# Optimization experiments

Hardware: AMD Instinct MI355X
Metric: run time of the kernel (lower is better)

Reference implementation:

```python
import jax, jax.numpy as jnp
import numpy as np

VOCAB, EMBED, H = 32000, 128, 128
B, T = 32, 2048


def setup_inputs() -> dict:
    key = jax.random.key(0)
    ks = jax.random.split(key, 8)
    tokens = jax.random.randint(ks[0], (B, T), 0, VOCAB, dtype=jnp.int32)
    emb = jax.random.normal(ks[1], (VOCAB, EMBED), jnp.float32) * 0.05
    # layer 0: input EMBED -> H ; layer 1: H -> H
    Wx0 = jax.random.normal(ks[2], (EMBED, H), jnp.float32) * (1.0 / np.sqrt(EMBED))
    Wh0 = jax.random.normal(ks[3], (H, H), jnp.float32) * (1.0 / np.sqrt(H))
    b0 = jnp.zeros((H,), jnp.float32)
    Wx1 = jax.random.normal(ks[4], (H, H), jnp.float32) * (1.0 / np.sqrt(H))
    Wh1 = jax.random.normal(ks[5], (H, H), jnp.float32) * (1.0 / np.sqrt(H))
    b1 = jnp.zeros((H,), jnp.float32)
    return {"tokens": tokens, "emb": emb, "Wx0": Wx0, "Wh0": Wh0, "b0": b0,
            "Wx1": Wx1, "Wh1": Wh1, "b1": b1}


def _simple_rnn(x, mask, Wx, Wh, b):
    # x: [B,T,Din], mask: [B,T] bool. Keras masked-step semantics: at masked
    # steps, state (== output for SimpleRNN) carries over unchanged.
    xt = jnp.swapaxes(x, 0, 1)                 # [T,B,Din]
    xproj = xt @ Wx + b                        # precompute input projection [T,B,H]
    mt = jnp.swapaxes(mask, 0, 1)[..., None]   # [T,B,1]
    h0 = jnp.zeros((x.shape[0], Wh.shape[0]), x.dtype)

    def step(h, inp):
        xp, m = inp
        h_new = jnp.tanh(xp + h @ Wh)
        h = jnp.where(m, h_new, h)
        return h, h

    _, ys = jax.lax.scan(step, h0, (xproj, mt))
    return jnp.swapaxes(ys, 0, 1)              # [B,T,H]


def reference(tokens, emb, Wx0, Wh0, b0, Wx1, Wh1, b1):
    mask = tokens != 0                          # mask_zero=True
    x = emb[tokens]                             # [B,T,E]
    x = _simple_rnn(x, mask, Wx0, Wh0, b0)
    x = _simple_rnn(x, mask, Wx1, Wh1, b1)
    return x
```

## Files before the change

### kernel.cpp

```cpp
#include <hip/hip_runtime.h>
#include <math.h>

#define BB 32
#define TT 2048
#define HH 128

#define LDS_BARRIER() asm volatile("s_waitcnt lgkmcnt(0)\n\ts_barrier" ::: "memory")

#define QPERM_F(v, CTRL)                                                      \
  __int_as_float(__builtin_amdgcn_update_dpp(                                 \
      0, __float_as_int(v), (CTRL), 0xF, 0xF, true))

template <bool GATHER>
__global__ __launch_bounds__(256) void proj_kernel(
    const float* __restrict__ src, const int* __restrict__ tokens,
    const float* __restrict__ W, const float* __restrict__ bias,
    float* __restrict__ out) {
  const int tid = threadIdx.x;
  const int jj = tid & 31;
  const int rr = tid >> 5;
  const int base = blockIdx.x * 64;

  __shared__ __align__(16) float srow[64][HH];
  __shared__ int stok[64];

  if (GATHER) {
    if (tid < 64) stok[tid] = tokens[base + tid];
    __syncthreads();
  }

#pragma unroll
  for (int i = 0; i < 8; ++i) {
    int idx = tid + i * 256;
    int row = idx >> 5;
    int c4 = idx & 31;
    const float* s = GATHER ? (src + (size_t)stok[row] * HH)
                            : (src + (size_t)(base + row) * HH);
    *(float4*)&srow[row][c4 * 4] = *(const float4*)&s[c4 * 4];
  }
  __syncthreads();

  float4 b4 = *(const float4*)&bias[jj * 4];
  float4 acc[8];
#pragma unroll
  for (int i = 0; i < 8; ++i) acc[i] = b4;

  for (int k = 0; k < HH; ++k) {
    float4 w4 = *(const float4*)&W[k * HH + jj * 4];
#pragma unroll
    for (int i = 0; i < 8; ++i) {
      float e = srow[rr * 8 + i][k];
      acc[i].x += e * w4.x;
      acc[i].y += e * w4.y;
      acc[i].z += e * w4.z;
      acc[i].w += e * w4.w;
    }
  }

#pragma unroll
  for (int i = 0; i < 8; ++i) {
    int row = base + rr * 8 + i;
    *(float4*)&out[(size_t)row * HH + jj * 4] = acc[i];
  }
}

__global__ __launch_bounds__(512) void rnn_kernel(
    float* io, const float* __restrict__ Wh, const int* __restrict__ tokens) {
  const int b = blockIdx.x;
  const int tid = threadIdx.x;
  const int j = tid >> 2;
  const int p = tid & 3;
  const int lane = tid & 63;

  float w[32];
#pragma unroll
  for (int c = 0; c < 32; ++c) {
    int k = 16 * (c >> 2) + 4 * p + (c & 3);
    w[c] = Wh[k * HH + j];
  }

  const int* tok = tokens + b * TT;
  unsigned bits = 0;
#pragma unroll
  for (int i = 0; i < 8; ++i) {
    int4 tk = *(const int4*)&tok[lane * 32 + i * 4];
    bits |= (unsigned)(tk.x != 0) << (i * 4 + 0);
    bits |= (unsigned)(tk.y != 0) << (i * 4 + 1);
    bits |= (unsigned)(tk.z != 0) << (i * 4 + 2);
    bits |= (unsigned)(tk.w != 0) << (i * 4 + 3);
  }

  __shared__ __align__(16) float hs[2][HH];
  if (tid < HH) hs[0][tid] = 0.0f;

  float* xp = io + (size_t)b * TT * HH;

  float h = 0.0f;
  float xcur = xp[(size_t)p * HH + j];
  LDS_BARRIER();

#define RNN_STEP(Q)                                                           \
  {                                                                           \
    const int t = t0 + (Q);                                                   \
    const float* hb = hs[t & 1];                                              \
    float a0 = 0.f, a1 = 0.f, a2 = 0.f, a3 = 0.f;                             \
    _Pragma("unroll") for (int i = 0; i < 8; ++i) {                           \
      float4 hv = *(const float4*)&hb[16 * i + 4 * p];                        \
      a0 += hv.x * w[4 * i + 0];                                              \
      a1 += hv.y * w[4 * i + 1];                                              \
      a2 += hv.z * w[4 * i + 2];                                              \
      a3 += hv.w * w[4 * i + 3];                                              \
    }                                                                         \
    float acc = (a0 + a1) + (a2 + a3);                                        \
    acc += QPERM_F(acc, 0xB1);                                     \
    acc += QPERM_F(acc, 0x4E);                                     \
    float x = QPERM_F(xcur, (Q)*0x55);             \
    float s = acc + x;                                                        \
    unsigned word =                                                           \
        (unsigned)__builtin_amdgcn_readlane((int)bits, t >> 5);               \
    int m = (word >> (t & 31)) & 1;                                           \
    float ax = fabsf(s);                                                      \
    float e = __expf(-2.0f * ax);                                             \
    float th = (1.0f - e) * __builtin_amdgcn_rcpf(1.0f + e);                  \
    th = copysignf(th, s);                                                    \
    h = m ? th : h;                                                           \
    if (p == 0) {                                                             \
      xp[(size_t)t * HH + j] = h;                   \
      hs[(t + 1) & 1][j] = h;                                  \
    }                                                                         \
    LDS_BARRIER();                                                            \
  }

  for (int t0 = 0; t0 < TT; t0 += 4) {
    float xnext = 0.0f;
    if (t0 + 4 < TT) xnext = xp[(size_t)(t0 + 4 + p) * HH + j];
    RNN_STEP(0)
    RNN_STEP(1)
    RNN_STEP(2)
    RNN_STEP(3)
    xcur = xnext;
  }
#undef RNN_STEP
}

extern "C" void kernel_launch(void* const* d_in, const int* in_sizes, int n_in,
                              void* d_out, int out_size, void* d_ws,
                              size_t ws_size, hipStream_t stream) {
  const int* tokens = (const int*)d_in[0];
  const float* emb = (const float*)d_in[1];
  const float* Wx0 = (const float*)d_in[2];
  const float* Wh0 = (const float*)d_in[3];
  const float* b0 = (const float*)d_in[4];
  const float* Wx1 = (const float*)d_in[5];
  const float* Wh1 = (const float*)d_in[6];
  const float* b1 = (const float*)d_in[7];
  float* out = (float*)d_out;
  float* ws = (float*)d_ws;

  const int rows = BB * TT;
  const int proj_blocks = rows / 64;

  proj_kernel<true><<<proj_blocks, 256, 0, stream>>>(emb, tokens, Wx0, b0, ws);
  rnn_kernel<<<BB, 512, 0, stream>>>(ws, Wh0, tokens);
  proj_kernel<false><<<proj_blocks, 256, 0, stream>>>(ws, nullptr, Wx1, b1, out);
  rnn_kernel<<<BB, 512, 0, stream>>>(out, Wh1, tokens);
}
```

Before: 1.412 ms.

## Fuse both RNN layers into one wavefront-skewed recurrent kernel

Replaces the two sequential RNN launches and the layer-1 projection with a single kernel. Layer 1 runs one step behind layer 0, and its input projection is folded into the per-step matvec using Wx1 held in registers. This halves the number of serial barrier-bound timesteps and drops the intermediate projection pass and its global round trip. In exchange each step does three matvecs with 256 threads, uses packed float2 FMAs, a padded LDS layout and an 8-lane reduction with a swizzle, and needs much higher register pressure (96 f32x2 weights per thread).

```diff
diff --git a/kernel.cpp b/kernel.cpp
--- a/kernel.cpp
+++ b/kernel.cpp
@@ -5,11 +5,28 @@
 #define TT 2048
 #define HH 128
 
+typedef float f32x2 __attribute__((ext_vector_type(2)));
+
 #define LDS_BARRIER() asm volatile("s_waitcnt lgkmcnt(0)\n\ts_barrier" ::: "memory")
 
 #define QPERM_F(v, CTRL)                                                      \
   __int_as_float(__builtin_amdgcn_update_dpp(                                 \
       0, __float_as_int(v), (CTRL), 0xF, 0xF, true))
+
+__device__ __forceinline__ float red8(float a) {
+  a += QPERM_F(a, 0xB1);
+  a += QPERM_F(a, 0x4E);
+  a += __int_as_float(
+      __builtin_amdgcn_ds_swizzle(__float_as_int(a), 0x101F));
+  return a;
+}
+
+__device__ __forceinline__ float tanh_fast(float s) {
+  float ax = fabsf(s);
+  float e = __expf(-2.0f * ax);
+  float th = (1.0f - e) * __builtin_amdgcn_rcpf(1.0f + e);
+  return copysignf(th, s);
+}
 
 template <bool GATHER>
 __global__ __launch_bounds__(256) void proj_kernel(
@@ -64,20 +81,30 @@
   }
 }
 
-__global__ __launch_bounds__(512) void rnn_kernel(
-    float* io, const float* __restrict__ Wh, const int* __restrict__ tokens) {
+__global__ __launch_bounds__(256, 1) void rnn_fused_kernel(
+    const float* __restrict__ xp0, float* __restrict__ out,
+    const float* __restrict__ Wh0, const float* __restrict__ Wx1,
+    const float* __restrict__ Wh1, const float* __restrict__ b1,
+    const int* __restrict__ tokens) {
   const int b = blockIdx.x;
   const int tid = threadIdx.x;
-  const int j = tid >> 2;
-  const int p = tid & 3;
   const int lane = tid & 63;
-
-  float w[32];
-#pragma unroll
-  for (int c = 0; c < 32; ++c) {
-    int k = 16 * (c >> 2) + 4 * p + (c & 3);
-    w[c] = Wh[k * HH + j];
-  }
+  const int p = lane & 7;
+  const int jgg = (lane >> 3) + ((tid >> 6) << 3);
+  const int col = 4 * jgg;
+
+  f32x2 w0a[16], w0b[16], wxa[16], wxb[16], wha[16], whb[16];
+#pragma unroll
+  for (int i = 0; i < 16; ++i) {
+    int row = 16 * p + i;
+    w0a[i] = *(const f32x2*)&Wh0[row * HH + col];
+    w0b[i] = *(const f32x2*)&Wh0[row * HH + col + 2];
+    wxa[i] = *(const f32x2*)&Wx1[row * HH + col];
+    wxb[i] = *(const f32x2*)&Wx1[row * HH + col + 2];
+    wha[i] = *(const f32x2*)&Wh1[row * HH + col];
+    whb[i] = *(const f32x2*)&Wh1[row * HH + col + 2];
+  }
+  const float4 bias = *(const float4*)&b1[col];
 
   const int* tok = tokens + b * TT;
   unsigned bits = 0;
@@ -90,57 +117,135 @@
     bits |= (unsigned)(tk.w != 0) << (i * 4 + 3);
   }
 
-  __shared__ __align__(16) float hs[2][HH];
-  if (tid < HH) hs[0][tid] = 0.0f;
-
-  float* xp = io + (size_t)b * TT * HH;
-
-  float h = 0.0f;
-  float xcur = xp[(size_t)p * HH + j];
+  __shared__ __align__(16) float h0s[2][160];
+  __shared__ __align__(16) float h1s[2][160];
+  if (tid < 160) {
+    h0s[0][tid] = 0.0f;
+    h1s[0][tid] = 0.0f;
+  }
+
+  const float* xp = xp0 + (size_t)b * TT * HH;
+  float* outp = out + (size_t)b * TT * HH;
+
+  float h0c0 = 0.f, h0c1 = 0.f, h0c2 = 0.f, h0c3 = 0.f;
+  float h1c0 = 0.f, h1c1 = 0.f, h1c2 = 0.f, h1c3 = 0.f;
+
+  float4 xcur = *(const float4*)&xp[col];
   LDS_BARRIER();
 
-#define RNN_STEP(Q)                                                           \
-  {                                                                           \
-    const int t = t0 + (Q);                                                   \
-    const float* hb = hs[t & 1];                                              \
-    float a0 = 0.f, a1 = 0.f, a2 = 0.f, a3 = 0.f;                             \
-    _Pragma("unroll") for (int i = 0; i < 8; ++i) {                           \
-      float4 hv = *(const float4*)&hb[16 * i + 4 * p];                        \
-      a0 += hv.x * w[4 * i + 0];                                              \
-      a1 += hv.y * w[4 * i + 1];                                              \
-      a2 += hv.z * w[4 * i + 2];                                              \
-      a3 += hv.w * w[4 * i + 3];                                              \
-    }                                                                         \
-    float acc = (a0 + a1) + (a2 + a3);                                        \
-    acc += QPERM_F(acc, 0xB1);                                     \
-    acc += QPERM_F(acc, 0x4E);                                     \
-    float x = QPERM_F(xcur, (Q)*0x55);             \
-    float s = acc + x;                                                        \
-    unsigned word =                                                           \
-        (unsigned)__builtin_amdgcn_readlane((int)bits, t >> 5);               \
-    int m = (word >> (t & 31)) & 1;                                           \
-    float ax = fabsf(s);                                                      \
-    float e = __expf(-2.0f * ax);                                             \
-    float th = (1.0f - e) * __builtin_amdgcn_rcpf(1.0f + e);                  \
-    th = copysignf(th, s);                                                    \
-    h = m ? th : h;                                                           \
-    if (p == 0) {                                                             \
-      xp[(size_t)t * HH + j] = h;                   \
-      hs[(t + 1) & 1][j] = h;                                  \
-    }                                                                         \
-    LDS_BARRIER();                                                            \
-  }
-
-  for (int t0 = 0; t0 < TT; t0 += 4) {
-    float xnext = 0.0f;
-    if (t0 + 4 < TT) xnext = xp[(size_t)(t0 + 4 + p) * HH + j];
-    RNN_STEP(0)
-    RNN_STEP(1)
-    RNN_STEP(2)
-    RNN_STEP(3)
-    xcur = xnext;
-  }
-#undef RNN_STEP
+  for (int t = 0; t < TT; ++t) {
+    float4 xn = make_float4(0.f, 0.f, 0.f, 0.f);
+    if (t + 1 < TT) xn = *(const float4*)&xp[(size_t)(t + 1) * HH + col];
+
+    const int pr = t & 1;
+    const int pw = pr ^ 1;
+    const float* hb0 = h0s[pr];
+    const float* hb1 = h1s[pr];
+
+    f32x2 a0a = {0.f, 0.f}, a0b = {0.f, 0.f};
+    f32x2 a1a = {0.f, 0.f}, a1b = {0.f, 0.f};
+
+#define K1(HV0, HV1, idx)                                                     \
+  a0a += (HV0)*w0a[idx];                                                      \
+  a0b += (HV0)*w0b[idx];                                                      \
+  a1a += (HV0)*wxa[idx];                                                      \
+  a1b += (HV0)*wxb[idx];                                                      \
+  a1a += (HV1)*wha[idx];                                                      \
+  a1b += (HV1)*whb[idx];
+
+#pragma unroll
+    for (int c = 0; c < 4; ++c) {
+      float4 hv0 = *(const float4*)&hb0[p * 20 + c * 4];
+      float4 hv1 = *(const float4*)&hb1[p * 20 + c * 4];
+      K1(hv0.x, hv1.x, c * 4 + 0)
+      K1(hv0.y, hv1.y, c * 4 + 1)
+      K1(hv0.z, hv1.z, c * 4 + 2)
+      K1(hv0.w, hv1.w, c * 4 + 3)
+    }
+#undef K1
+
+    float s00 = red8(a0a.x) + xcur.x;
+    float s01 = red8(a0a.y) + xcur.y;
+    float s02 = red8(a0b.x) + xcur.z;
+    float s03 = red8(a0b.y) + xcur.w;
+    float s10 = red8(a1a.x) + bias.x;
+    float s11 = red8(a1a.y) + bias.y;
+    float s12 = red8(a1b.x) + bias.z;
+    float s13 = red8(a1b.y) + bias.w;
+
+    unsigned wd0 = (unsigned)__builtin_amdgcn_readlane((int)bits, t >> 5);
+    int m0 = (wd0 >> (t & 31)) & 1;
+    if (m0) {
+      h0c0 = tanh_fast(s00);
+      h0c1 = tanh_fast(s01);
+      h0c2 = tanh_fast(s02);
+      h0c3 = tanh_fast(s03);
+    }
+    int m1 = 0;
+    if (t > 0) {
+      int t1 = t - 1;
+      unsigned wd1 = (unsigned)__builtin_amdgcn_readlane((int)bits, t1 >> 5);
+      m1 = (wd1 >> (t1 & 31)) & 1;
+    }
+    if (m1) {
+      h1c0 = tanh_fast(s10);
+      h1c1 = tanh_fast(s11);
+      h1c2 = tanh_fast(s12);
+      h1c3 = tanh_fast(s13);
+    }
+
+    if ((lane & 7) == 0) {
+      const int widx = (jgg >> 2) * 20 + (jgg & 3) * 4;
+      *(float4*)&h0s[pw][widx] = make_float4(h0c0, h0c1, h0c2, h0c3);
+      *(float4*)&h1s[pw][widx] = make_float4(h1c0, h1c1, h1c2, h1c3);
+      if (t > 0)
+        *(float4*)&outp[(size_t)(t - 1) * HH + col] =
+            make_float4(h1c0, h1c1, h1c2, h1c3);
+    }
+    LDS_BARRIER();
+    xcur = xn;
+  }
+
+  {
+    const float* hb0 = h0s[0];
+    const float* hb1 = h1s[0];
+    f32x2 a1a = {0.f, 0.f}, a1b = {0.f, 0.f};
+
+#define K1T(HV0, HV1, idx)                                                    \
+  a1a += (HV0)*wxa[idx];                                                      \
+  a1b += (HV0)*wxb[idx];                                                      \
+  a1a += (HV1)*wha[idx];                                                      \
+  a1b += (HV1)*whb[idx];
+
+#pragma unroll
+    for (int c = 0; c < 4; ++c) {
+      float4 hv0 = *(const float4*)&hb0[p * 20 + c * 4];
+      float4 hv1 = *(const float4*)&hb1[p * 20 + c * 4];
+      K1T(hv0.x, hv1.x, c * 4 + 0)
+      K1T(hv0.y, hv1.y, c * 4 + 1)
+      K1T(hv0.z, hv1.z, c * 4 + 2)
+      K1T(hv0.w, hv1.w, c * 4 + 3)
+    }
+#undef K1T
+
+    float s10 = red8(a1a.x) + bias.x;
+    float s11 = red8(a1a.y) + bias.y;
+    float s12 = red8(a1b.x) + bias.z;
+    float s13 = red8(a1b.y) + bias.w;
+
+    const int t1 = TT - 1;
+    unsigned wd1 = (unsigned)__builtin_amdgcn_readlane((int)bits, t1 >> 5);
+    int m1 = (wd1 >> (t1 & 31)) & 1;
+    if (m1) {
+      h1c0 = tanh_fast(s10);
+      h1c1 = tanh_fast(s11);
+      h1c2 = tanh_fast(s12);
+      h1c3 = tanh_fast(s13);
+    }
+    if ((lane & 7) == 0)
+      *(float4*)&outp[(size_t)t1 * HH + col] =
+          make_float4(h1c0, h1c1, h1c2, h1c3);
+  }
 }
 
 extern "C" void kernel_launch(void* const* d_in, const int* in_sizes, int n_in,
@@ -161,7 +266,5 @@
   const int proj_blocks = rows / 64;
 
   proj_kernel<true><<<proj_blocks, 256, 0, stream>>>(emb, tokens, Wx0, b0, ws);
-  rnn_kernel<<<BB, 512, 0, stream>>>(ws, Wh0, tokens);
-  proj_kernel<false><<<proj_blocks, 256, 0, stream>>>(ws, nullptr, Wx1, b1, out);
-  rnn_kernel<<<BB, 512, 0, stream>>>(out, Wh1, tokens);
-}
+  rnn_fused_kernel<<<BB, 256, 0, stream>>>(ws, out, Wh0, Wx1, Wh1, b1, tokens);
+}
```

After: 1.557 ms. 10.3% more time.

## Fuse both RNN layers into one wavefront-pipelined recurrent kernel

Applied to the files above, without the earlier changes.

Replaces the layer-0 recurrence, the layer-1 input projection and the layer-1 recurrence with a single kernel. Layer 1 runs one timestep behind layer 0, and its input projection is computed per step from the layer-0 hidden state held in LDS. Weights for all three matrices are kept in registers, and partial sums are reduced across lanes with DPP and swizzle. This removes one projection launch and two full-sequence DRAM round trips, and it halves the number of serial step barriers. In exchange each step does more arithmetic and reduction work, and register pressure rises sharply.

```diff
diff --git a/kernel.cpp b/kernel.cpp
--- a/kernel.cpp
+++ b/kernel.cpp
@@ -5,11 +5,38 @@
 #define TT 2048
 #define HH 128
 
+typedef float f32x2 __attribute__((ext_vector_type(2)));
+
 #define LDS_BARRIER() asm volatile("s_waitcnt lgkmcnt(0)\n\ts_barrier" ::: "memory")
 
 #define QPERM_F(v, CTRL)                                                      \
   __int_as_float(__builtin_amdgcn_update_dpp(                                 \
       0, __float_as_int(v), (CTRL), 0xF, 0xF, true))
+
+template <int OFFS>
+__device__ __forceinline__ float swz_xor(float v) {
+  return __int_as_float(__builtin_amdgcn_ds_swizzle(__float_as_int(v), OFFS));
+}
+
+#define MERGE_DPP(x, y, bit, CTRL)                                            \
+  ({                                                                          \
+    float _k = (bit) ? (y) : (x);                                             \
+    float _s = (bit) ? (x) : (y);                                             \
+    _k + QPERM_F(_s, CTRL);                                                   \
+  })
+#define MERGE_SWZ(x, y, bit, OFFS)                                            \
+  ({                                                                          \
+    float _k = (bit) ? (y) : (x);                                             \
+    float _s = (bit) ? (x) : (y);                                             \
+    _k + swz_xor<OFFS>(_s);                                                   \
+  })
+
+__device__ __forceinline__ float tanh_fast(float s) {
+  float ax = fabsf(s);
+  float e = __expf(-2.0f * ax);
+  float th = (1.0f - e) * __builtin_amdgcn_rcpf(1.0f + e);
+  return copysignf(th, s);
+}
 
 template <bool GATHER>
 __global__ __launch_bounds__(256) void proj_kernel(
@@ -64,20 +91,36 @@
   }
 }
 
-__global__ __launch_bounds__(512) void rnn_kernel(
-    float* io, const float* __restrict__ Wh, const int* __restrict__ tokens) {
+__global__ __launch_bounds__(512, 1) void rnn_fused_kernel(
+    const float* __restrict__ xp0, float* __restrict__ out,
+    const float* __restrict__ Wh0, const float* __restrict__ Wx1,
+    const float* __restrict__ Wh1, const float* __restrict__ bias1,
+    const int* __restrict__ tokens) {
   const int b = blockIdx.x;
   const int tid = threadIdx.x;
-  const int j = tid >> 2;
-  const int p = tid & 3;
   const int lane = tid & 63;
-
-  float w[32];
-#pragma unroll
-  for (int c = 0; c < 32; ++c) {
-    int k = 16 * (c >> 2) + 4 * p + (c & 3);
-    w[c] = Wh[k * HH + j];
-  }
+  const int lb0 = lane & 1;
+  const int lb1 = (lane >> 1) & 1;
+  const int lb2 = (lane >> 2) & 1;
+  const int lb3 = (lane >> 3) & 1;
+  const int p = lane & 15;
+  const int jg = tid >> 4;
+  const int colbase = jg * 4;
+  const int kbase = p * 8;
+  const int mycol = colbase + 2 * lb1 + lb0;
+
+  f32x2 w0a[8], w0b[8], wxa[8], wxb[8], wha[8], whb[8];
+#pragma unroll
+  for (int kk = 0; kk < 8; ++kk) {
+    int row = kbase + kk;
+    w0a[kk] = *(const f32x2*)&Wh0[row * HH + colbase];
+    w0b[kk] = *(const f32x2*)&Wh0[row * HH + colbase + 2];
+    wxa[kk] = *(const f32x2*)&Wx1[row * HH + colbase];
+    wxb[kk] = *(const f32x2*)&Wx1[row * HH + colbase + 2];
+    wha[kk] = *(const f32x2*)&Wh1[row * HH + colbase];
+    whb[kk] = *(const f32x2*)&Wh1[row * HH + colbase + 2];
+  }
+  const float biasv = bias1[mycol];
 
   const int* tok = tokens + b * TT;
   unsigned bits = 0;
@@ -90,57 +133,132 @@
     bits |= (unsigned)(tk.w != 0) << (i * 4 + 3);
   }
 
-  __shared__ __align__(16) float hs[2][HH];
-  if (tid < HH) hs[0][tid] = 0.0f;
-
-  float* xp = io + (size_t)b * TT * HH;
+  __shared__ __align__(16) float h0s[2][160];
+  __shared__ __align__(16) float h1s[2][160];
+  if (tid < 160) {
+    h0s[0][tid] = 0.0f;
+    h1s[0][tid] = 0.0f;
+  }
+
+  const float* xp = xp0 + (size_t)b * TT * HH + mycol;
+  float* outp = out + (size_t)b * TT * HH + mycol;
+
+  const int roff = (p >> 1) * 20 + (p & 1) * 8;
+  const int wslot = (mycol >> 4) * 20 + (mycol & 15);
 
   float h = 0.0f;
-  float xcur = xp[(size_t)p * HH + j];
+  float xc = xp[0];
+  float xn = xp[HH];
   LDS_BARRIER();
 
-#define RNN_STEP(Q)                                                           \
-  {                                                                           \
-    const int t = t0 + (Q);                                                   \
-    const float* hb = hs[t & 1];                                              \
-    float a0 = 0.f, a1 = 0.f, a2 = 0.f, a3 = 0.f;                             \
-    _Pragma("unroll") for (int i = 0; i < 8; ++i) {                           \
-      float4 hv = *(const float4*)&hb[16 * i + 4 * p];                        \
-      a0 += hv.x * w[4 * i + 0];                                              \
-      a1 += hv.y * w[4 * i + 1];                                              \
-      a2 += hv.z * w[4 * i + 2];                                              \
-      a3 += hv.w * w[4 * i + 3];                                              \
-    }                                                                         \
-    float acc = (a0 + a1) + (a2 + a3);                                        \
-    acc += QPERM_F(acc, 0xB1);                                     \
-    acc += QPERM_F(acc, 0x4E);                                     \
-    float x = QPERM_F(xcur, (Q)*0x55);             \
-    float s = acc + x;                                                        \
-    unsigned word =                                                           \
-        (unsigned)__builtin_amdgcn_readlane((int)bits, t >> 5);               \
-    int m = (word >> (t & 31)) & 1;                                           \
-    float ax = fabsf(s);                                                      \
-    float e = __expf(-2.0f * ax);                                             \
-    float th = (1.0f - e) * __builtin_amdgcn_rcpf(1.0f + e);                  \
-    th = copysignf(th, s);                                                    \
-    h = m ? th : h;                                                           \
-    if (p == 0) {                                                             \
-      xp[(size_t)t * HH + j] = h;                   \
-      hs[(t + 1) & 1][j] = h;                                  \
-    }                                                                         \
-    LDS_BARRIER();                                                            \
-  }
-
-  for (int t0 = 0; t0 < TT; t0 += 4) {
-    float xnext = 0.0f;
-    if (t0 + 4 < TT) xnext = xp[(size_t)(t0 + 4 + p) * HH + j];
-    RNN_STEP(0)
-    RNN_STEP(1)
-    RNN_STEP(2)
-    RNN_STEP(3)
-    xcur = xnext;
-  }
-#undef RNN_STEP
+  for (int t = 0; t < TT; ++t) {
+    const int pr = t & 1;
+    const int pw = pr ^ 1;
+    const float* hb0 = &h0s[pr][roff];
+    const float* hb1 = &h1s[pr][roff];
+    float4 hA0 = *(const float4*)&hb0[0];
+    float4 hB0 = *(const float4*)&hb0[4];
+    float4 hA1 = *(const float4*)&hb1[0];
+    float4 hB1 = *(const float4*)&hb1[4];
+
+    float x2 = 0.0f;
+    if (t + 2 < TT) x2 = xp[(size_t)(t + 2) * HH];
+
+    f32x2 a0a = {0.f, 0.f}, a0b = {0.f, 0.f};
+    f32x2 a1a = {0.f, 0.f}, a1b = {0.f, 0.f};
+#define KS(H0, H1, kk)                                                        \
+  a0a += (H0)*w0a[kk];                                                        \
+  a0b += (H0)*w0b[kk];                                                        \
+  a1a += (H0)*wxa[kk];                                                        \
+  a1b += (H0)*wxb[kk];                                                        \
+  a1a += (H1)*wha[kk];                                                        \
+  a1b += (H1)*whb[kk];
+    KS(hA0.x, hA1.x, 0)
+    KS(hA0.y, hA1.y, 1)
+    KS(hA0.z, hA1.z, 2)
+    KS(hA0.w, hA1.w, 3)
+    KS(hB0.x, hB1.x, 4)
+    KS(hB0.y, hB1.y, 5)
+    KS(hB0.z, hB1.z, 6)
+    KS(hB0.w, hB1.w, 7)
+#undef KS
+
+    float m0 = MERGE_DPP(a0a.x, a0a.y, lb0, 0xB1);
+    float m1 = MERGE_DPP(a0b.x, a0b.y, lb0, 0xB1);
+    float m2 = MERGE_DPP(a1a.x, a1a.y, lb0, 0xB1);
+    float m3 = MERGE_DPP(a1b.x, a1b.y, lb0, 0xB1);
+    float n0 = MERGE_DPP(m0, m1, lb1, 0x4E);
+    float n1 = MERGE_DPP(m2, m3, lb1, 0x4E);
+    float r = MERGE_SWZ(n0, n1, lb2, 0x101F);
+    r += QPERM_F(r, 0x128);
+
+    float s = r + (lb2 ? biasv : xc);
+
+    unsigned wd0 = (unsigned)__builtin_amdgcn_readlane((int)bits, t >> 5);
+    int mk0 = (wd0 >> (t & 31)) & 1;
+    int mk1 = 0;
+    if (t > 0) {
+      unsigned wd1 =
+          (unsigned)__builtin_amdgcn_readlane((int)bits, (t - 1) >> 5);
+      mk1 = (wd1 >> ((t - 1) & 31)) & 1;
+    }
+    int mm = lb2 ? mk1 : mk0;
+    float th = tanh_fast(s);
+    h = mm ? th : h;
+
+    if (!lb3) {
+      if (lb2) {
+        h1s[pw][wslot] = h;
+        if (t > 0) outp[(size_t)(t - 1) * HH] = h;
+      } else {
+        h0s[pw][wslot] = h;
+      }
+    }
+    LDS_BARRIER();
+    xc = xn;
+    xn = x2;
+  }
+
+  {
+    const float* hb0 = &h0s[0][roff];
+    const float* hb1 = &h1s[0][roff];
+    float4 hA0 = *(const float4*)&hb0[0];
+    float4 hB0 = *(const float4*)&hb0[4];
+    float4 hA1 = *(const float4*)&hb1[0];
+    float4 hB1 = *(const float4*)&hb1[4];
+
+    f32x2 a1a = {0.f, 0.f}, a1b = {0.f, 0.f};
+#define KT(H0, H1, kk)                                                        \
+  a1a += (H0)*wxa[kk];                                                        \
+  a1b += (H0)*wxb[kk];                                                        \
+  a1a += (H1)*wha[kk];                                                        \
+  a1b += (H1)*whb[kk];
+    KT(hA0.x, hA1.x, 0)
+    KT(hA0.y, hA1.y, 1)
+    KT(hA0.z, hA1.z, 2)
+    KT(hA0.w, hA1.w, 3)
+    KT(hB0.x, hB1.x, 4)
+    KT(hB0.y, hB1.y, 5)
+    KT(hB0.z, hB1.z, 6)
+    KT(hB0.w, hB1.w, 7)
+#undef KT
+
+    float m2 = MERGE_DPP(a1a.x, a1a.y, lb0, 0xB1);
+    float m3 = MERGE_DPP(a1b.x, a1b.y, lb0, 0xB1);
+    float n1 = MERGE_DPP(m2, m3, lb1, 0x4E);
+    float r = n1 + swz_xor<0x101F>(n1);
+    r += QPERM_F(r, 0x128);
+    float s = r + biasv;
+
+    const int t1 = TT - 1;
+    unsigned wd1 = (unsigned)__builtin_amdgcn_readlane((int)bits, t1 >> 5);
+    int mk1 = (wd1 >> (t1 & 31)) & 1;
+    if (lb2) {
+      float th = tanh_fast(s);
+      float hv = mk1 ? th : h;
+      if (!lb3) outp[(size_t)t1 * HH] = hv;
+    }
+  }
 }
 
 extern "C" void kernel_launch(void* const* d_in, const int* in_sizes, int n_in,
@@ -161,7 +279,5 @@
   const int proj_blocks = rows / 64;
 
   proj_kernel<true><<<proj_blocks, 256, 0, stream>>>(emb, tokens, Wx0, b0, ws);
-  rnn_kernel<<<BB, 512, 0, stream>>>(ws, Wh0, tokens);
-  proj_kernel<false><<<proj_blocks, 256, 0, stream>>>(ws, nullptr, Wx1, b1, out);
-  rnn_kernel<<<BB, 512, 0, stream>>>(out, Wh1, tokens);
-}
+  rnn_fused_kernel<<<BB, 512, 0, stream>>>(ws, out, Wh0, Wx1, Wh1, b1, tokens);
+}
```

Result: faster. 1.227 ms (-13.1%).

## Fuse both RNN layers and second projection into one wavefront-pipelined kernel

Applied to the files above, without the earlier changes.

Replaces the layer-0 recurrence, the layer-1 input projection and the layer-1 recurrence with a single kernel. At each step it advances layer 0 at time t and layer 1 at time t-1, skewed by one step. Each thread now holds slices of Wh0, Wx1 and Wh1 in registers, and the K-reduction is done with a DPP/swizzle merge tree over 32 lanes. This removes one full sequential pass over T, a projection launch, and the round trip of the intermediate activations through global memory. In exchange it uses 1024-thread blocks, more register pressure and a longer reduction chain per step.

```diff
diff --git a/kernel.cpp b/kernel.cpp
--- a/kernel.cpp
+++ b/kernel.cpp
@@ -5,11 +5,38 @@
 #define TT 2048
 #define HH 128
 
+typedef float f32x2 __attribute__((ext_vector_type(2)));
+
 #define LDS_BARRIER() asm volatile("s_waitcnt lgkmcnt(0)\n\ts_barrier" ::: "memory")
 
 #define QPERM_F(v, CTRL)                                                      \
   __int_as_float(__builtin_amdgcn_update_dpp(                                 \
       0, __float_as_int(v), (CTRL), 0xF, 0xF, true))
+
+template <int OFFS>
+__device__ __forceinline__ float swz_xor(float v) {
+  return __int_as_float(__builtin_amdgcn_ds_swizzle(__float_as_int(v), OFFS));
+}
+
+#define MERGE_DPP(x, y, bit, CTRL)                                            \
+  ({                                                                          \
+    float _k = (bit) ? (y) : (x);                                             \
+    float _s = (bit) ? (x) : (y);                                             \
+    _k + QPERM_F(_s, CTRL);                                                   \
+  })
+#define MERGE_SWZ(x, y, bit, OFFS)                                            \
+  ({                                                                          \
+    float _k = (bit) ? (y) : (x);                                             \
+    float _s = (bit) ? (x) : (y);                                             \
+    _k + swz_xor<OFFS>(_s);                                                   \
+  })
+
+__device__ __forceinline__ float tanh_fast(float s) {
+  float ax = fabsf(s);
+  float e = __expf(-2.0f * ax);
+  float th = (1.0f - e) * __builtin_amdgcn_rcpf(1.0f + e);
+  return copysignf(th, s);
+}
 
 template <bool GATHER>
 __global__ __launch_bounds__(256) void proj_kernel(
@@ -64,20 +91,37 @@
   }
 }
 
-__global__ __launch_bounds__(512) void rnn_kernel(
-    float* io, const float* __restrict__ Wh, const int* __restrict__ tokens) {
+__global__ __launch_bounds__(1024)
+__attribute__((amdgpu_waves_per_eu(4, 4))) void rnn_fused_kernel(
+    const float* __restrict__ xp0, float* __restrict__ out,
+    const float* __restrict__ Wh0, const float* __restrict__ Wx1,
+    const float* __restrict__ Wh1, const float* __restrict__ bias1,
+    const int* __restrict__ tokens) {
   const int b = blockIdx.x;
   const int tid = threadIdx.x;
-  const int j = tid >> 2;
-  const int p = tid & 3;
   const int lane = tid & 63;
-
-  float w[32];
-#pragma unroll
-  for (int c = 0; c < 32; ++c) {
-    int k = 16 * (c >> 2) + 4 * p + (c & 3);
-    w[c] = Wh[k * HH + j];
-  }
+  const int p = tid & 31;
+  const int jg = tid >> 5;
+  const int lb0 = p & 1;
+  const int lb1 = (p >> 1) & 1;
+  const int lb2 = (p >> 2) & 1;
+  const int mycol = 4 * jg + 2 * lb1 + lb0;
+
+  f32x2 w0a[4], w0b[4], wxa[4], wxb[4], wha[4], whb[4];
+#pragma unroll
+  for (int i = 0; i < 4; ++i) {
+    int row = 4 * p + i;
+    float4 v0 = *(const float4*)&Wh0[row * HH + 4 * jg];
+    float4 v1 = *(const float4*)&Wx1[row * HH + 4 * jg];
+    float4 v2 = *(const float4*)&Wh1[row * HH + 4 * jg];
+    w0a[i] = (f32x2){v0.x, v0.y};
+    w0b[i] = (f32x2){v0.z, v0.w};
+    wxa[i] = (f32x2){v1.x, v1.y};
+    wxb[i] = (f32x2){v1.z, v1.w};
+    wha[i] = (f32x2){v2.x, v2.y};
+    whb[i] = (f32x2){v2.z, v2.w};
+  }
+  const float biasv = bias1[mycol];
 
   const int* tok = tokens + b * TT;
   unsigned bits = 0;
@@ -90,57 +134,112 @@
     bits |= (unsigned)(tk.w != 0) << (i * 4 + 3);
   }
 
-  __shared__ __align__(16) float hs[2][HH];
-  if (tid < HH) hs[0][tid] = 0.0f;
-
-  float* xp = io + (size_t)b * TT * HH;
+  __shared__ __align__(16) float h0s[2][HH];
+  __shared__ __align__(16) float h1s[2][HH];
+  if (tid < HH) {
+    h0s[0][tid] = 0.0f;
+    h1s[0][tid] = 0.0f;
+  }
+
+  const float* xp = xp0 + (size_t)b * TT * HH + mycol;
+  float* outp = out + (size_t)b * TT * HH + mycol;
 
   float h = 0.0f;
-  float xcur = xp[(size_t)p * HH + j];
+  float xc = xp[0];
+  float xn = xp[HH];
   LDS_BARRIER();
 
-#define RNN_STEP(Q)                                                           \
+#define RNN_STEP(HRD0, HRD1, HWR0, HWR1, T, XC)                               \
   {                                                                           \
-    const int t = t0 + (Q);                                                   \
-    const float* hb = hs[t & 1];                                              \
-    float a0 = 0.f, a1 = 0.f, a2 = 0.f, a3 = 0.f;                             \
-    _Pragma("unroll") for (int i = 0; i < 8; ++i) {                           \
-      float4 hv = *(const float4*)&hb[16 * i + 4 * p];                        \
-      a0 += hv.x * w[4 * i + 0];                                              \
-      a1 += hv.y * w[4 * i + 1];                                              \
-      a2 += hv.z * w[4 * i + 2];                                              \
-      a3 += hv.w * w[4 * i + 3];                                              \
+    float4 q = *(const float4*)&(HRD0)[4 * p];                                \
+    float4 g = *(const float4*)&(HRD1)[4 * p];                                \
+    f32x2 a0a = {0.f, 0.f}, a0b = {0.f, 0.f};                                 \
+    f32x2 a1a = {0.f, 0.f}, a1b = {0.f, 0.f};                                 \
+    a0a += q.x * w0a[0]; a0b += q.x * w0b[0];                                 \
+    a1a += q.x * wxa[0]; a1b += q.x * wxb[0];                                 \
+    a1a += g.x * wha[0]; a1b += g.x * whb[0];                                 \
+    a0a += q.y * w0a[1]; a0b += q.y * w0b[1];                                 \
+    a1a += q.y * wxa[1]; a1b += q.y * wxb[1];                                 \
+    a1a += g.y * wha[1]; a1b += g.y * whb[1];                                 \
+    a0a += q.z * w0a[2]; a0b += q.z * w0b[2];                                 \
+    a1a += q.z * wxa[2]; a1b += q.z * wxb[2];                                 \
+    a1a += g.z * wha[2]; a1b += g.z * whb[2];                                 \
+    a0a += q.w * w0a[3]; a0b += q.w * w0b[3];                                 \
+    a1a += q.w * wxa[3]; a1b += q.w * wxb[3];                                 \
+    a1a += g.w * wha[3]; a1b += g.w * whb[3];                                 \
+    float m0 = MERGE_DPP(a0a.x, a0a.y, lb0, 0xB1);                            \
+    float m1 = MERGE_DPP(a0b.x, a0b.y, lb0, 0xB1);                            \
+    float m2 = MERGE_DPP(a1a.x, a1a.y, lb0, 0xB1);                            \
+    float m3 = MERGE_DPP(a1b.x, a1b.y, lb0, 0xB1);                            \
+    float n0 = MERGE_DPP(m0, m1, lb1, 0x4E);                                  \
+    float n1 = MERGE_DPP(m2, m3, lb1, 0x4E);                                  \
+    float r = MERGE_SWZ(n0, n1, lb2, 0x101F);               \
+    r += QPERM_F(r, 0x128);                              \
+    r += swz_xor<0x401F>(r);                                       \
+    float s = r + (lb2 ? biasv : (XC));                                       \
+    unsigned wd0 = (unsigned)__builtin_amdgcn_readlane((int)bits, (T) >> 5);  \
+    int mk0 = (wd0 >> ((T)&31)) & 1;                                          \
+    int mk1 = 0;                                                              \
+    if ((T) > 0) {                                                            \
+      unsigned wd1 =                                                          \
+          (unsigned)__builtin_amdgcn_readlane((int)bits, ((T)-1) >> 5);       \
+      mk1 = (wd1 >> (((T)-1) & 31)) & 1;                                      \
     }                                                                         \
-    float acc = (a0 + a1) + (a2 + a3);                                        \
-    acc += QPERM_F(acc, 0xB1);                                     \
-    acc += QPERM_F(acc, 0x4E);                                     \
-    float x = QPERM_F(xcur, (Q)*0x55);             \
-    float s = acc + x;                                                        \
-    unsigned word =                                                           \
-        (unsigned)__builtin_amdgcn_readlane((int)bits, t >> 5);               \
-    int m = (word >> (t & 31)) & 1;                                           \
-    float ax = fabsf(s);                                                      \
-    float e = __expf(-2.0f * ax);                                             \
-    float th = (1.0f - e) * __builtin_amdgcn_rcpf(1.0f + e);                  \
-    th = copysignf(th, s);                                                    \
-    h = m ? th : h;                                                           \
-    if (p == 0) {                                                             \
-      xp[(size_t)t * HH + j] = h;                   \
-      hs[(t + 1) & 1][j] = h;                                  \
+    int mm = lb2 ? mk1 : mk0;                                                 \
+    float th = tanh_fast(s);                                                  \
+    h = mm ? th : h;                                                          \
+    if ((p & 24) == 0) {                      \
+      if (lb2) {                                                              \
+        (HWR1)[mycol] = h;                               \
+        if ((T) > 0) outp[(size_t)((T)-1) * HH] = h;                          \
+      } else {                                                                \
+        (HWR0)[mycol] = h;                                 \
+      }                                                                       \
     }                                                                         \
     LDS_BARRIER();                                                            \
   }
 
-  for (int t0 = 0; t0 < TT; t0 += 4) {
-    float xnext = 0.0f;
-    if (t0 + 4 < TT) xnext = xp[(size_t)(t0 + 4 + p) * HH + j];
-    RNN_STEP(0)
-    RNN_STEP(1)
-    RNN_STEP(2)
-    RNN_STEP(3)
-    xcur = xnext;
+  for (int t0 = 0; t0 < TT; t0 += 2) {
+    float x2 = 0.0f, x3 = 0.0f;
+    if (t0 + 2 < TT) x2 = xp[(size_t)(t0 + 2) * HH];
+    if (t0 + 3 < TT) x3 = xp[(size_t)(t0 + 3) * HH];
+    RNN_STEP(h0s[0], h1s[0], h0s[1], h1s[1], t0, xc)
+    RNN_STEP(h0s[1], h1s[1], h0s[0], h1s[0], t0 + 1, xn)
+    xc = x2;
+    xn = x3;
   }
 #undef RNN_STEP
+
+  {
+    float4 q = *(const float4*)&h0s[0][4 * p];
+    float4 g = *(const float4*)&h1s[0][4 * p];
+    f32x2 a1a = {0.f, 0.f}, a1b = {0.f, 0.f};
+    a1a += q.x * wxa[0]; a1b += q.x * wxb[0];
+    a1a += g.x * wha[0]; a1b += g.x * whb[0];
+    a1a += q.y * wxa[1]; a1b += q.y * wxb[1];
+    a1a += g.y * wha[1]; a1b += g.y * whb[1];
+    a1a += q.z * wxa[2]; a1b += q.z * wxb[2];
+    a1a += g.z * wha[2]; a1b += g.z * whb[2];
+    a1a += q.w * wxa[3]; a1b += q.w * wxb[3];
+    a1a += g.w * wha[3]; a1b += g.w * whb[3];
+
+    float m2 = MERGE_DPP(a1a.x, a1a.y, lb0, 0xB1);
+    float m3 = MERGE_DPP(a1b.x, a1b.y, lb0, 0xB1);
+    float n1 = MERGE_DPP(m2, m3, lb1, 0x4E);
+    float r = n1 + swz_xor<0x101F>(n1);
+    r += QPERM_F(r, 0x128);
+    r += swz_xor<0x401F>(r);
+    float s = r + biasv;
+
+    const int t1 = TT - 1;
+    unsigned wd1 = (unsigned)__builtin_amdgcn_readlane((int)bits, t1 >> 5);
+    int mk1 = (wd1 >> (t1 & 31)) & 1;
+    if (lb2) {
+      float th = tanh_fast(s);
+      float hv = mk1 ? th : h;
+      if ((p & 24) == 0) outp[(size_t)t1 * HH] = hv;
+    }
+  }
 }
 
 extern "C" void kernel_launch(void* const* d_in, const int* in_sizes, int n_in,
@@ -161,7 +260,6 @@
   const int proj_blocks = rows / 64;
 
   proj_kernel<true><<<proj_blocks, 256, 0, stream>>>(emb, tokens, Wx0, b0, ws);
-  rnn_kernel<<<BB, 512, 0, stream>>>(ws, Wh0, tokens);
-  proj_kernel<false><<<proj_blocks, 256, 0, stream>>>(ws, nullptr, Wx1, b1, out);
-  rnn_kernel<<<BB, 512, 0, stream>>>(out, Wh1, tokens);
-}
+  rnn_fused_kernel<<<BB, 1024, 0, stream>>>(ws, out, Wh0, Wx1, Wh1, b1,
+                                            tokens);
+}
```

After: 1.507 ms. 1.07x slower.
